# Kernel optimization log

Hardware: AMD Instinct MI355X
Metric: run time of the kernel (lower is better)

## Reference

```python
import jax, jax.numpy as jnp
import numpy as np

N = 100000      # nodes
E = 1600000     # edges (avg degree 16)
D_IN = 128; D_HID = 128; D_OUT = 64; ATT = 64
G = 64          # number of graphs in the batch (dgl.mean_nodes pooling)


def setup_inputs() -> dict:
    key = jax.random.key(0)
    ks = jax.random.split(key, 24)
    def p(i, shape, scale=0.05):
        return jax.random.normal(ks[i], shape, dtype=jnp.float32) * scale
    return dict(
        x=jax.random.normal(ks[0], (N, D_IN), dtype=jnp.float32),
        edge_src=jax.random.randint(ks[1], (E,), 0, N),
        edge_dst=jax.random.randint(ks[2], (E,), 0, N),
        edge_w=jax.random.uniform(ks[3], (E,), dtype=jnp.float32),
        graph_ids=jnp.sort(jax.random.randint(ks[4], (N,), 0, G)),
        # layer 1 (HeteAggregateLayer for type 'node')
        w_self1=p(5, (D_IN, D_HID)), w_rel1=p(6, (D_IN, D_HID)), bias1=p(7, (1, D_HID)),
        w_q1=p(8, (D_HID, ATT)), w_k1=p(9, (D_HID, ATT)), w_att1=p(10, (2 * ATT, 1)),
        # layer 2
        w_self2=p(11, (D_HID, D_OUT)), w_rel2=p(12, (D_HID, D_OUT)), bias2=p(13, (1, D_OUT)),
        w_q2=p(14, (D_OUT, ATT)), w_k2=p(15, (D_OUT, ATT)), w_att2=p(16, (2 * ATT, 1)),
        # final MLP: Linear(d, d//2) -> ReLU -> Linear(d//2, 1)
        mlp_w1=p(17, (D_OUT, D_OUT // 2)), mlp_b1=p(18, (D_OUT // 2,)),
        mlp_w2=p(19, (D_OUT // 2, 1)), mlp_b2=p(20, (1,)),
    )


def _spmm(src, dst, w, feat):
    # torch.spmm(adj, feat): out[dst] += w_edge * feat[src]
    return jax.ops.segment_sum(feat[src] * w[:, None], dst, num_segments=N)


def _agg(x, src, dst, ew, w_self, w_rel, bias, w_q, w_k, w_att):
    self_ft = x @ w_self                        # [N, D]
    nb_ft = _spmm(src, dst, ew, x @ w_rel)      # [N, D]
    nb = jnp.stack([self_ft, nb_ft])            # [T=2, N, D] (self first, as in torch cat order)
    q = self_ft @ w_q                           # [N, A] query (repeated across types)
    keys = jnp.einsum('tnd,da->tna', nb, w_k)   # [T, N, A]
    a = w_att[:, 0]
    # e = elu(cat([keys, query], -1) @ w_att); split w_att into key/query halves
    e = jax.nn.elu(keys @ a[:ATT] + q @ a[ATT:])  # [T, N]
    att = jax.nn.softmax(e, axis=0)               # softmax over types per node
    out = jnp.einsum('tn,tnd->nd', att, nb) + bias
    return out, att.T                              # attention returned as [N, T]


def reference(x, edge_src, edge_dst, edge_w, graph_ids,
              w_self1, w_rel1, bias1, w_q1, w_k1, w_att1,
              w_self2, w_rel2, bias2, w_q2, w_k2, w_att2,
              mlp_w1, mlp_b1, mlp_w2, mlp_b2):
    h, att1 = _agg(x, edge_src, edge_dst, edge_w,
                   w_self1, w_rel1, bias1, w_q1, w_k1, w_att1)
    h = jax.nn.elu(h)   # dropout(0.5) is identity in eval mode
    h, att2 = _agg(h, edge_src, edge_dst, edge_w,
                   w_self2, w_rel2, bias2, w_q2, w_k2, w_att2)
    # dgl.mean_nodes over the batched graph
    sums = jax.ops.segment_sum(h, graph_ids, num_segments=G)
    cnt = jax.ops.segment_sum(jnp.ones((N, 1), h.dtype), graph_ids, num_segments=G)
    hg = sums / jnp.maximum(cnt, 1.0)               # [G, D_OUT]
    hid = jax.nn.relu(hg @ mlp_w1 + mlp_b1)
    graph_embd = hid @ mlp_w2 + mlp_b2              # [G, 1]
    return graph_embd, att1, att2
```

## Files before the change

kernel.cpp:

```cpp
#include <hip/hip_runtime.h>
#include <hip/hip_bf16.h>
#include <cstdint>
#include <cstddef>

static constexpr int D_IN  = 128;
static constexpr int D_HID = 128;
static constexpr int D_OUT = 64;
static constexpr int ATTD  = 64;
static constexpr int NG    = 64;
static constexpr int NB    = 256;
static constexpr int NBLK  = 256;
static constexpr int BSHIFT = 9;

typedef __attribute__((ext_vector_type(8))) short s16x8;
typedef __attribute__((ext_vector_type(4))) float f32x4;
typedef unsigned short ushort_t;
typedef unsigned int uint_t;

__device__ __forceinline__ unsigned short bf_bits(float f) {
    union { __hip_bfloat16 h; unsigned short u; } cv;
    cv.h = __float2bfloat16(f);
    return cv.u;
}
__device__ __forceinline__ float bf_lo(uint_t v) { return __uint_as_float(v << 16); }
__device__ __forceinline__ float bf_hi(uint_t v) { return __uint_as_float(v & 0xffff0000u); }
__device__ __forceinline__ float bf_one(unsigned short u) { return __uint_as_float(((uint_t)u) << 16); }

template <int C, bool A32, bool OA_BF>
__device__ __forceinline__ void gemm_dual_body(ushort_t* wt, int bx,
        const void* __restrict__ A, int M,
        const ushort_t* __restrict__ WTa, const ushort_t* __restrict__ WTb,
        void* __restrict__ Oa, ushort_t* __restrict__ Ob) {
    constexpr int K = 128;
    constexpr int RS = K + 8;

    for (int idx = threadIdx.x; idx < 2 * C * (K / 8); idx += 256) {
        int half = idx >= C * (K / 8);
        int l = idx - half * C * (K / 8);
        int c  = l >> 4;
        int kc = l & 15;
        const ushort_t* W = half ? WTb : WTa;
        *(uint4*)&wt[half * C * RS + c * RS + kc * 8] = *(const uint4*)&W[c * K + kc * 8];
    }
    __syncthreads();

    const int w    = threadIdx.x >> 6;
    const int lane = threadIdx.x & 63;
    const int row  = bx * 64 + w * 16 + (lane & 15);
    const int rowc = row < M ? row : (M - 1);
    const int kb   = (lane >> 4) * 8;

    s16x8 afr[4];
    if (A32) {
        const float* Af = (const float*)A + (size_t)rowc * K + kb;
#pragma unroll
        for (int ks = 0; ks < 4; ++ks) {
            float4 f0 = *(const float4*)(Af + ks * 32);
            float4 f1 = *(const float4*)(Af + ks * 32 + 4);
            s16x8 a;
            a[0] = (short)bf_bits(f0.x); a[1] = (short)bf_bits(f0.y);
            a[2] = (short)bf_bits(f0.z); a[3] = (short)bf_bits(f0.w);
            a[4] = (short)bf_bits(f1.x); a[5] = (short)bf_bits(f1.y);
            a[6] = (short)bf_bits(f1.z); a[7] = (short)bf_bits(f1.w);
            afr[ks] = a;
        }
    } else {
        const ushort_t* Ab = (const ushort_t*)A + (size_t)rowc * K + kb;
#pragma unroll
        for (int ks = 0; ks < 4; ++ks) afr[ks] = *(const s16x8*)(Ab + ks * 32);
    }

    const int colc = lane & 15;
    const int r0   = bx * 64 + w * 16 + (lane >> 4) * 4;

#pragma unroll
    for (int z = 0; z < 2; ++z) {
        const ushort_t* wz = wt + z * C * RS;
#pragma unroll
        for (int ct = 0; ct < C / 16; ++ct) {
            f32x4 acc = {0.f, 0.f, 0.f, 0.f};
            const int colb = ct * 16 + colc;
#pragma unroll
            for (int ks = 0; ks < 4; ++ks) {
                s16x8 b = *(const s16x8*)&wz[colb * RS + ks * 32 + kb];
                acc = __builtin_amdgcn_mfma_f32_16x16x32_bf16(afr[ks], b, acc, 0, 0, 0);
            }
            if (z == 0) {
                if (OA_BF) {
                    ushort_t* O = (ushort_t*)Oa;
#pragma unroll
                    for (int j = 0; j < 4; ++j)
                        if (r0 + j < M) O[(size_t)(r0 + j) * C + colb] = bf_bits(acc[j]);
                } else {
                    float* O = (float*)Oa;
#pragma unroll
                    for (int j = 0; j < 4; ++j)
                        if (r0 + j < M) O[(size_t)(r0 + j) * C + colb] = acc[j];
                }
            } else {
#pragma unroll
                for (int j = 0; j < 4; ++j)
                    if (r0 + j < M) Ob[(size_t)(r0 + j) * C + colb] = bf_bits(acc[j]);
            }
        }
    }
}

__global__ __launch_bounds__(256) void gemm2_kernel(
        const void* __restrict__ A, int M,
        const ushort_t* __restrict__ WTa, const ushort_t* __restrict__ WTb,
        void* __restrict__ Oa, ushort_t* __restrict__ Ob) {
    __shared__ ushort_t wt[2 * 64 * 136];
    gemm_dual_body<64, false, false>(wt, blockIdx.x, A, M, WTa, WTb, Oa, Ob);
}

__global__ __launch_bounds__(256) void phaseA(
        const int* __restrict__ edst, int E, int chunk, int* __restrict__ bh,
        const float* __restrict__ w_self1, const float* __restrict__ w_rel1,
        const float* __restrict__ w_self2, const float* __restrict__ w_rel2,
        ushort_t* __restrict__ wtb,
        const float* __restrict__ w_q1, const float* __restrict__ w_k1,
        const float* __restrict__ w_att1,
        const float* __restrict__ w_q2, const float* __restrict__ w_k2,
        const float* __restrict__ w_att2,
        float* __restrict__ small, float* __restrict__ zero_region,
        int* __restrict__ dctr) {
    __shared__ int h[NB];
    int bid = blockIdx.x;
    if (bid < NBLK) {
        h[threadIdx.x] = 0;
        __syncthreads();
        int beg = bid * chunk;
        int end = min(E, beg + chunk);
        for (int i = beg + threadIdx.x; i < end; i += 256)
            atomicAdd(&h[edst[i] >> BSHIFT], 1);
        __syncthreads();
        bh[threadIdx.x * NBLK + bid] = h[threadIdx.x];
    } else if (bid < NBLK + 192) {
        int idx = (bid - NBLK) * 256 + threadIdx.x;
        const float* src; int base, Cc;
        if (idx < 16384)      { src = w_self1; base = 0;     Cc = 128; }
        else if (idx < 32768) { src = w_rel1;  base = 16384; Cc = 128; }
        else if (idx < 40960) { src = w_self2; base = 32768; Cc = 64;  }
        else                  { src = w_rel2;  base = 40960; Cc = 64;  }
        int l = idx - base;
        int c = l >> 7;
        int k = l & 127;
        wtb[base + l] = bf_bits(src[k * Cc + c]);
    } else if (bid < NBLK + 194) {
        int idx = (bid - NBLK - 192) * 256 + threadIdx.x;
        if (idx < 384) {
            float acc = 0.f;
            if (idx < 128) {
                int d = idx;
                for (int a = 0; a < ATTD; ++a) acc += w_k1[d * ATTD + a] * w_att1[a];
                small[0 + d] = acc;
            } else if (idx < 256) {
                int d = idx - 128;
                for (int a = 0; a < ATTD; ++a) acc += w_q1[d * ATTD + a] * w_att1[ATTD + a];
                small[128 + d] = acc;
            } else if (idx < 320) {
                int d = idx - 256;
                for (int a = 0; a < ATTD; ++a) acc += w_k2[d * ATTD + a] * w_att2[a];
                small[256 + d] = acc;
            } else {
                int d = idx - 320;
                for (int a = 0; a < ATTD; ++a) acc += w_q2[d * ATTD + a] * w_att2[ATTD + a];
                small[320 + d] = acc;
            }
        }
    } else {
        for (int i = threadIdx.x; i < NG * D_OUT + NG; i += 256) zero_region[i] = 0.f;
        if (threadIdx.x == 0) *dctr = 0;
    }
}

__global__ __launch_bounds__(256) void scanA(int* __restrict__ bh,
        int* __restrict__ bt, int* __restrict__ bb, int* __restrict__ dctr) {
    __shared__ int wsum[4];
    __shared__ int lastFlag;
    const int t = blockIdx.x;
    const int i = threadIdx.x;
    if (i == 0) lastFlag = 0;
    int v = bh[t * NBLK + i];
    int lane = i & 63, w = i >> 6;
    int incl = v;
#pragma unroll
    for (int off = 1; off < 64; off <<= 1) {
        int u = __shfl_up(incl, off);
        if (lane >= off) incl += u;
    }
    if (lane == 63) wsum[w] = incl;
    __syncthreads();
    int wbase = 0;
#pragma unroll
    for (int k = 0; k < 4; ++k) if (k < w) wbase += wsum[k];
    int excl = wbase + incl - v;
    bh[t * NBLK + i] = excl;
    __syncthreads();
    if (i == 255) {
        atomicExch(&bt[t], excl + v);
        __threadfence();
        int old = atomicAdd(dctr, 1);
        if (old == NBLK - 1) lastFlag = 1;
    }
    __syncthreads();
    if (lastFlag) {
        int vb = atomicAdd(&bt[i], 0);
        int incl2 = vb;
#pragma unroll
        for (int off = 1; off < 64; off <<= 1) {
            int u = __shfl_up(incl2, off);
            if (lane >= off) incl2 += u;
        }
        if (lane == 63) wsum[w] = incl2;
        __syncthreads();
        int wb2 = 0;
#pragma unroll
        for (int k = 0; k < 4; ++k) if (k < w) wb2 += wsum[k];
        int excl2 = wb2 + incl2 - vb;
        bb[i] = excl2;
        if (i == 255) bb[256] = excl2 + vb;
    }
}

__global__ __launch_bounds__(256) void phaseB(
        const int* __restrict__ src, const int* __restrict__ dst,
        const float* __restrict__ ew, int E, int chunk,
        const int* __restrict__ bh, const int* __restrict__ bb,
        uint2* __restrict__ part,
        const float* __restrict__ x, int M,
        const ushort_t* __restrict__ wt_s1, const ushort_t* __restrict__ wt_r1,
        void* __restrict__ Oa, ushort_t* __restrict__ Ob) {
    __shared__ ushort_t smem[2 * 128 * 136];
    int bid = blockIdx.x;
    if (bid < NBLK) {
        int* ofs = (int*)smem;
        ofs[threadIdx.x] = bh[threadIdx.x * NBLK + bid] + bb[threadIdx.x];
        __syncthreads();
        int beg = bid * chunk;
        int end = min(E, beg + chunk);
        for (int i = beg + threadIdx.x; i < end; i += 256) {
            int d = dst[i];
            int b = d >> BSHIFT;
            int pos = atomicAdd(&ofs[b], 1);
            part[pos] = make_uint2((uint_t)src[i] | ((uint_t)(d & 511) << 20),
                                   __float_as_uint(ew[i]));
        }
    } else {
        gemm_dual_body<128, true, true>(smem, bid - NBLK, x, M, wt_s1, wt_r1, Oa, Ob);
    }
}

__global__ __launch_bounds__(256) void phaseC(
        const uint2* __restrict__ part, const int* __restrict__ bb,
        int* __restrict__ rowptr, float2* __restrict__ sorted, int N_, int nbuck,
        int g1,
        const float* __restrict__ x, int M,
        const ushort_t* __restrict__ wt_s1, const ushort_t* __restrict__ wt_r1,
        void* __restrict__ Oa, ushort_t* __restrict__ Ob) {
    __shared__ ushort_t smem[2 * 128 * 136];
    int bid = blockIdx.x;
    if (bid >= nbuck) {
        gemm_dual_body<128, true, true>(smem, g1 + (bid - nbuck), x, M, wt_s1, wt_r1, Oa, Ob);
        return;
    }
    int* hist = (int*)smem;
    int* wsum = (int*)smem + 512;
    int b = bid;
    int t = threadIdx.x;
    int start = bb[b], end = bb[b + 1];
    hist[t] = 0; hist[t + 256] = 0;
    __syncthreads();
    {
        int i = start + t;
        for (; i + 1792 < end; i += 2048) {
            int k[8];
#pragma unroll
            for (int j = 0; j < 8; ++j) k[j] = part[i + j * 256].x >> 20;
#pragma unroll
            for (int j = 0; j < 8; ++j) atomicAdd(&hist[k[j]], 1);
        }
        for (; i < end; i += 256) atomicAdd(&hist[part[i].x >> 20], 1);
    }
    __syncthreads();
    int v0 = hist[2 * t], v1 = hist[2 * t + 1];
    int pair = v0 + v1;
    int lane = t & 63, w = t >> 6;
    int incl = pair;
#pragma unroll
    for (int off = 1; off < 64; off <<= 1) {
        int u = __shfl_up(incl, off);
        if (lane >= off) incl += u;
    }
    if (lane == 63) wsum[w] = incl;
    __syncthreads();
    int wbase = 0;
#pragma unroll
    for (int i = 0; i < 4; ++i) if (i < w) wbase += wsum[i];
    int excl = wbase + incl - pair;
    __syncthreads();
    hist[2 * t]     = start + excl;
    hist[2 * t + 1] = start + excl + v0;
    int dst0 = (b << BSHIFT) + 2 * t;
    if (dst0 < N_)     rowptr[dst0]     = start + excl + v0;
    if (dst0 + 1 < N_) rowptr[dst0 + 1] = start + excl + v0 + v1;
    __syncthreads();
    {
        int i = start + t;
        for (; i + 1792 < end; i += 2048) {
            uint2 r[8];
#pragma unroll
            for (int j = 0; j < 8; ++j) r[j] = part[i + j * 256];
#pragma unroll
            for (int j = 0; j < 8; ++j) {
                int dl = r[j].x >> 20;
                int pos = atomicAdd(&hist[dl], 1);
                sorted[pos] = make_float2(__int_as_float((int)(r[j].x & 0xFFFFF)),
                                          __uint_as_float(r[j].y));
            }
        }
        for (; i < end; i += 256) {
            uint2 r = part[i];
            int dl = r.x >> 20;
            int pos = atomicAdd(&hist[dl], 1);
            sorted[pos] = make_float2(__int_as_float((int)(r.x & 0xFFFFF)),
                                      __uint_as_float(r.y));
        }
    }
}

__global__ __launch_bounds__(256) void fused1(
        const uint_t* __restrict__ selfp, const ushort_t* __restrict__ relft,
        const int* __restrict__ rowptr, const float2* __restrict__ sorted,
        const float* __restrict__ vk, const float* __restrict__ vq,
        const float* __restrict__ bias,
        uint_t* __restrict__ hout, float* __restrict__ attout, int M) {
    const int wv   = __builtin_amdgcn_readfirstlane(threadIdx.x >> 6);
    const int lane = threadIdx.x & 63;
    const int n = blockIdx.x * 4 + wv;
    if (n >= M) return;

    uint_t s2 = selfp[(size_t)n * 64 + lane];
    float sv0 = bf_lo(s2), sv1 = bf_hi(s2);
    float nb0 = 0.f, nb1 = 0.f;

    const int beg = (n > 0) ? rowptr[n - 1] : 0;
    const int end = rowptr[n];
    const int len = end - beg;
    const char* base = (const char*)relft;
    const uint_t lb = (uint_t)lane << 2;

    int e = beg;
    const int efull = beg + (len & ~7);
    for (; e < efull; e += 8) {
        float2 swb[8];
#pragma unroll
        for (int j = 0; j < 8; ++j) swb[j] = sorted[e + j];
        uint_t vv[8];
#pragma unroll
        for (int j = 0; j < 8; ++j)
            vv[j] = *(const uint_t*)(base + (((uint_t)__float_as_uint(swb[j].x) << 8) | lb));
#pragma unroll
        for (int j = 0; j < 8; ++j) {
            nb0 = fmaf(swb[j].y, bf_lo(vv[j]), nb0);
            nb1 = fmaf(swb[j].y, bf_hi(vv[j]), nb1);
        }
    }
    if (e < end) {
        float2 swb[8];
        float  wb[8];
#pragma unroll
        for (int j = 0; j < 8; ++j) {
            int idx = e + j;
            int cl  = idx < end ? idx : e;
            swb[j] = sorted[cl];
            wb[j]  = idx < end ? swb[j].y : 0.f;
        }
        uint_t vv[8];
#pragma unroll
        for (int j = 0; j < 8; ++j)
            vv[j] = *(const uint_t*)(base + (((uint_t)__float_as_uint(swb[j].x) << 8) | lb));
#pragma unroll
        for (int j = 0; j < 8; ++j) {
            nb0 = fmaf(wb[j], bf_lo(vv[j]), nb0);
            nb1 = fmaf(wb[j], bf_hi(vv[j]), nb1);
        }
    }

    float2 k2 = ((const float2*)vk)[lane];
    float2 q2 = ((const float2*)vq)[lane];
    float sk = sv0 * k2.x + sv1 * k2.y;
    float sq = sv0 * q2.x + sv1 * q2.y;
    float nk = nb0 * k2.x + nb1 * k2.y;
#pragma unroll
    for (int off = 32; off; off >>= 1) {
        sk += __shfl_xor(sk, off);
        sq += __shfl_xor(sq, off);
        nk += __shfl_xor(nk, off);
    }
    float e0 = sk + sq;
    float e1 = nk + sq;
    e0 = e0 > 0.f ? e0 : expm1f(e0);
    e1 = e1 > 0.f ? e1 : expm1f(e1);
    float m = fmaxf(e0, e1);
    float a0 = expf(e0 - m);
    float a1 = expf(e1 - m);
    float inv = 1.f / (a0 + a1);
    a0 *= inv; a1 *= inv;

    float2 b2 = ((const float2*)bias)[lane];
    float o0 = fmaf(a0, sv0, fmaf(a1, nb0, b2.x));
    float o1 = fmaf(a0, sv1, fmaf(a1, nb1, b2.y));
    o0 = o0 > 0.f ? o0 : expm1f(o0);
    o1 = o1 > 0.f ? o1 : expm1f(o1);
    hout[(size_t)n * 64 + lane] = (uint_t)bf_bits(o0) | ((uint_t)bf_bits(o1) << 16);
    if (lane == 0) {
        attout[2 * (size_t)n + 0] = a0;
        attout[2 * (size_t)n + 1] = a1;
    }
}

__global__ __launch_bounds__(256) void fused2(
        const float* __restrict__ selfp, const ushort_t* __restrict__ relft,
        const int* __restrict__ rowptr, const float2* __restrict__ sorted,
        const float* __restrict__ vk, const float* __restrict__ vq,
        const float* __restrict__ bias,
        float* __restrict__ hout, float* __restrict__ attout, int M) {
    const int wv   = __builtin_amdgcn_readfirstlane(threadIdx.x >> 6);
    const int lane = threadIdx.x & 63;
    const int n = blockIdx.x * 4 + wv;
    if (n >= M) return;

    float sv = selfp[(size_t)n * 64 + lane];
    float nb = 0.f;

    const int beg = (n > 0) ? rowptr[n - 1] : 0;
    const int end = rowptr[n];
    const int len = end - beg;
    const char* base = (const char*)relft;
    const uint_t lb = (uint_t)lane << 1;

    int e = beg;
    const int efull = beg + (len & ~7);
    for (; e < efull; e += 8) {
        float2 swb[8];
#pragma unroll
        for (int j = 0; j < 8; ++j) swb[j] = sorted[e + j];
        ushort_t vv[8];
#pragma unroll
        for (int j = 0; j < 8; ++j)
            vv[j] = *(const ushort_t*)(base + (((uint_t)__float_as_uint(swb[j].x) << 7) | lb));
#pragma unroll
        for (int j = 0; j < 8; ++j) nb = fmaf(swb[j].y, bf_one(vv[j]), nb);
    }
    if (e < end) {
        float2 swb[8];
        float  wb[8];
#pragma unroll
        for (int j = 0; j < 8; ++j) {
            int idx = e + j;
            int cl  = idx < end ? idx : e;
            swb[j] = sorted[cl];
            wb[j]  = idx < end ? swb[j].y : 0.f;
        }
        ushort_t vv[8];
#pragma unroll
        for (int j = 0; j < 8; ++j)
            vv[j] = *(const ushort_t*)(base + (((uint_t)__float_as_uint(swb[j].x) << 7) | lb));
#pragma unroll
        for (int j = 0; j < 8; ++j) nb = fmaf(wb[j], bf_one(vv[j]), nb);
    }

    float kk = vk[lane], qq = vq[lane];
    float sk = sv * kk;
    float sq = sv * qq;
    float nk = nb * kk;
#pragma unroll
    for (int off = 32; off; off >>= 1) {
        sk += __shfl_xor(sk, off);
        sq += __shfl_xor(sq, off);
        nk += __shfl_xor(nk, off);
    }
    float e0 = sk + sq;
    float e1 = nk + sq;
    e0 = e0 > 0.f ? e0 : expm1f(e0);
    e1 = e1 > 0.f ? e1 : expm1f(e1);
    float m = fmaxf(e0, e1);
    float a0 = expf(e0 - m);
    float a1 = expf(e1 - m);
    float inv = 1.f / (a0 + a1);
    a0 *= inv; a1 *= inv;

    hout[(size_t)n * 64 + lane] = fmaf(a0, sv, fmaf(a1, nb, bias[lane]));
    if (lane == 0) {
        attout[2 * (size_t)n + 0] = a0;
        attout[2 * (size_t)n + 1] = a1;
    }
}

__global__ __launch_bounds__(256) void pool_sum_v2(
        const float* __restrict__ h, const int* __restrict__ gid,
        float* __restrict__ sums, float* __restrict__ cnt, int M, int chunk) {
    int wave = threadIdx.x >> 6;
    int lane = threadIdx.x & 63;
    int wid  = blockIdx.x * 4 + wave;
    int beg  = wid * chunk;
    int end  = min(M, beg + chunk);
    if (beg >= end) return;

    int   cur_g = gid[beg];
    float acc   = 0.f;
    int   cl    = 0;
    for (int n = beg; n < end; ++n) {
        int g = gid[n];
        if (g != cur_g) {
            atomicAdd(&sums[(size_t)cur_g * D_OUT + lane], acc);
            if (lane == 0) atomicAdd(&cnt[cur_g], (float)cl);
            cur_g = g; acc = 0.f; cl = 0;
        }
        acc += h[(size_t)n * D_OUT + lane];
        ++cl;
    }
    atomicAdd(&sums[(size_t)cur_g * D_OUT + lane], acc);
    if (lane == 0) atomicAdd(&cnt[cur_g], (float)cl);
}

__global__ void pool_mlp(const float* __restrict__ sums, const float* __restrict__ cnt,
                         const float* __restrict__ w1, const float* __restrict__ b1,
                         const float* __restrict__ w2, const float* __restrict__ b2,
                         float* __restrict__ out) {
    int g = threadIdx.x;
    if (g >= NG) return;
    float c = fmaxf(cnt[g], 1.0f);
    float inv = 1.0f / c;
    float hg[D_OUT];
#pragma unroll
    for (int d = 0; d < D_OUT; ++d) hg[d] = sums[g * D_OUT + d] * inv;
    float acc = b2[0];
    for (int j = 0; j < D_OUT / 2; ++j) {
        float hid = b1[j];
#pragma unroll 8
        for (int d = 0; d < D_OUT; ++d) hid = fmaf(hg[d], w1[d * (D_OUT / 2) + j], hid);
        hid = fmaxf(hid, 0.f);
        acc = fmaf(hid, w2[j], acc);
    }
    out[g] = acc;
}

extern "C" void kernel_launch(void* const* d_in, const int* in_sizes, int n_in,
                              void* d_out, int out_size, void* d_ws, size_t ws_size,
                              hipStream_t stream) {
    const float* x       = (const float*)d_in[0];
    const int*   esrc    = (const int*)  d_in[1];
    const int*   edst    = (const int*)  d_in[2];
    const float* ew      = (const float*)d_in[3];
    const int*   gid     = (const int*)  d_in[4];
    const float* w_self1 = (const float*)d_in[5];
    const float* w_rel1  = (const float*)d_in[6];
    const float* bias1   = (const float*)d_in[7];
    const float* w_q1    = (const float*)d_in[8];
    const float* w_k1    = (const float*)d_in[9];
    const float* w_att1  = (const float*)d_in[10];
    const float* w_self2 = (const float*)d_in[11];
    const float* w_rel2  = (const float*)d_in[12];
    const float* bias2   = (const float*)d_in[13];
    const float* w_q2    = (const float*)d_in[14];
    const float* w_k2    = (const float*)d_in[15];
    const float* w_att2  = (const float*)d_in[16];
    const float* mlp_w1  = (const float*)d_in[17];
    const float* mlp_b1  = (const float*)d_in[18];
    const float* mlp_w2  = (const float*)d_in[19];
    const float* mlp_b2  = (const float*)d_in[20];

    const int N = in_sizes[0] / D_IN;
    const int E = in_sizes[1];

    float* out = (float*)d_out;
    float* out_embd = out;
    float* out_att1 = out + NG;
    float* out_att2 = out + NG + 2 * (size_t)N;

    float* ws = (float*)d_ws;
    size_t nf = (size_t)N;
    float* bufS = ws;
    float* bufR = ws + nf * 64;
    float* bufH = ws + nf * 128;
    uint2* part = (uint2*)bufH;
    int* ip     = (int*)(ws + nf * 192);
    int* bh     = ip;
    int* rowptr = ip + NB * NBLK;
    int* bb     = rowptr + N;
    int* bt     = bb + 257;
    int* dctr   = bt + 256;
    size_t int_end = nf * 192 + (size_t)NB * NBLK + nf + 257 + 256 + 1;
    int_end = (int_end + 1) & ~(size_t)1;
    float2* sorted = (float2*)(ws + int_end);
    float* small = ws + int_end + 2 * (size_t)E;
    float* vk1 = small + 0;
    float* vq1 = small + 128;
    float* vk2 = small + 256;
    float* vq2 = small + 320;
    float* sums = small + 384;
    float* cnt  = small + 384 + NG * D_OUT;
    ushort_t* wtb = (ushort_t*)(small + 384 + NG * D_OUT + NG);
    ushort_t* wt_s1 = wtb;
    ushort_t* wt_r1 = wtb + 16384;
    ushort_t* wt_s2 = wtb + 32768;
    ushort_t* wt_r2 = wtb + 40960;

    const int chunk = (E + NBLK - 1) / NBLK;
    const int nbuck = (N + (1 << BSHIFT) - 1) >> BSHIFT;
    const int nx    = (N + 63) / 64;
    const int g1    = (nx * 3) / 5;

    phaseA<<<NBLK + 192 + 2 + 1, 256, 0, stream>>>(
        edst, E, chunk, bh,
        w_self1, w_rel1, w_self2, w_rel2, wtb,
        w_q1, w_k1, w_att1, w_q2, w_k2, w_att2, small, sums, dctr);

    scanA<<<NBLK, 256, 0, stream>>>(bh, bt, bb, dctr);

    phaseB<<<NBLK + g1, 256, 0, stream>>>(
        esrc, edst, ew, E, chunk, bh, bb, part,
        x, N, wt_s1, wt_r1, (void*)bufS, (ushort_t*)bufR);

    phaseC<<<nbuck + (nx - g1), 256, 0, stream>>>(
        part, bb, rowptr, sorted, N, nbuck, g1,
        x, N, wt_s1, wt_r1, (void*)bufS, (ushort_t*)bufR);

    fused1<<<(N + 3) / 4, 256, 0, stream>>>(
        (const uint_t*)bufS, (const ushort_t*)bufR, rowptr, sorted,
        vk1, vq1, bias1, (uint_t*)bufH, out_att1, N);

    gemm2_kernel<<<nx, 256, 0, stream>>>(
        (const void*)bufH, N, wt_s2, wt_r2, (void*)bufS, (ushort_t*)bufR);

    fused2<<<(N + 3) / 4, 256, 0, stream>>>(
        bufS, (const ushort_t*)bufR, rowptr, sorted,
        vk2, vq2, bias2, bufH, out_att2, N);

    {
        int pblocks = 1024;
        int pchunk  = (N + pblocks * 4 - 1) / (pblocks * 4);
        pool_sum_v2<<<pblocks, 256, 0, stream>>>(bufH, gid, sums, cnt, N, pchunk);
    }
    pool_mlp<<<1, 64, 0, stream>>>(sums, cnt, mlp_w1, mlp_b1, mlp_w2, mlp_b2, out_embd);
}
```

Baseline: 273.3 us.

## Store layer-2 self features as bf16, unroll edge loops, fuse pooling with MLP

The layer-2 GEMM now writes the self-projection in bf16 instead of fp32, and fused2 reads and widens it, which halves that buffer's traffic at some precision cost. The histogram and scatter loops in phaseA and phaseB are unrolled by four so several loads are in flight per thread. The pooling sum and final MLP are merged into one kernel, where the last block to finish (tracked by a new atomic counter reset in phaseA) computes the MLP. This removes one kernel launch but adds a grid-wide completion counter.

```diff
diff --git a/kernel.cpp b/kernel.cpp
--- a/kernel.cpp
+++ b/kernel.cpp
@@ -111,7 +111,7 @@
         const ushort_t* __restrict__ WTa, const ushort_t* __restrict__ WTb,
         void* __restrict__ Oa, ushort_t* __restrict__ Ob) {
     __shared__ ushort_t wt[2 * 64 * 136];
-    gemm_dual_body<64, false, false>(wt, blockIdx.x, A, M, WTa, WTb, Oa, Ob);
+    gemm_dual_body<64, false, true>(wt, blockIdx.x, A, M, WTa, WTb, Oa, Ob);
 }
 
 __global__ __launch_bounds__(256) void phaseA(
@@ -124,7 +124,7 @@
         const float* __restrict__ w_q2, const float* __restrict__ w_k2,
         const float* __restrict__ w_att2,
         float* __restrict__ small, float* __restrict__ zero_region,
-        int* __restrict__ dctr) {
+        int* __restrict__ dctr, int* __restrict__ dctr2) {
     __shared__ int h[NB];
     int bid = blockIdx.x;
     if (bid < NBLK) {
@@ -132,7 +132,15 @@
         __syncthreads();
         int beg = bid * chunk;
         int end = min(E, beg + chunk);
-        for (int i = beg + threadIdx.x; i < end; i += 256)
+        int i = beg + threadIdx.x;
+        for (; i + 768 < end; i += 1024) {
+            int d0 = edst[i], d1 = edst[i + 256], d2 = edst[i + 512], d3 = edst[i + 768];
+            atomicAdd(&h[d0 >> BSHIFT], 1);
+            atomicAdd(&h[d1 >> BSHIFT], 1);
+            atomicAdd(&h[d2 >> BSHIFT], 1);
+            atomicAdd(&h[d3 >> BSHIFT], 1);
+        }
+        for (; i < end; i += 256)
             atomicAdd(&h[edst[i] >> BSHIFT], 1);
         __syncthreads();
         bh[threadIdx.x * NBLK + bid] = h[threadIdx.x];
@@ -171,7 +179,7 @@
         }
     } else {
         for (int i = threadIdx.x; i < NG * D_OUT + NG; i += 256) zero_region[i] = 0.f;
-        if (threadIdx.x == 0) *dctr = 0;
+        if (threadIdx.x == 0) { *dctr = 0; *dctr2 = 0; }
     }
 }
 
@@ -240,7 +248,25 @@
         __syncthreads();
         int beg = bid * chunk;
         int end = min(E, beg + chunk);
-        for (int i = beg + threadIdx.x; i < end; i += 256) {
+        int i = beg + threadIdx.x;
+        for (; i + 768 < end; i += 1024) {
+            int   d[4], s[4];
+            float wv[4];
+#pragma unroll
+            for (int j = 0; j < 4; ++j) d[j] = dst[i + j * 256];
+#pragma unroll
+            for (int j = 0; j < 4; ++j) s[j] = src[i + j * 256];
+#pragma unroll
+            for (int j = 0; j < 4; ++j) wv[j] = ew[i + j * 256];
+#pragma unroll
+            for (int j = 0; j < 4; ++j) {
+                int b = d[j] >> BSHIFT;
+                int pos = atomicAdd(&ofs[b], 1);
+                part[pos] = make_uint2((uint_t)s[j] | ((uint_t)(d[j] & 511) << 20),
+                                       __float_as_uint(wv[j]));
+            }
+        }
+        for (; i < end; i += 256) {
             int d = dst[i];
             int b = d >> BSHIFT;
             int pos = atomicAdd(&ofs[b], 1);
@@ -422,7 +448,7 @@
 }
 
 __global__ __launch_bounds__(256) void fused2(
-        const float* __restrict__ selfp, const ushort_t* __restrict__ relft,
+        const ushort_t* __restrict__ selfp, const ushort_t* __restrict__ relft,
         const int* __restrict__ rowptr, const float2* __restrict__ sorted,
         const float* __restrict__ vk, const float* __restrict__ vq,
         const float* __restrict__ bias,
@@ -432,7 +458,7 @@
     const int n = blockIdx.x * 4 + wv;
     if (n >= M) return;
 
-    float sv = selfp[(size_t)n * 64 + lane];
+    float sv = bf_one(selfp[(size_t)n * 64 + lane]);
     float nb = 0.f;
 
     const int beg = (n > 0) ? rowptr[n - 1] : 0;
@@ -499,53 +525,62 @@
     }
 }
 
-__global__ __launch_bounds__(256) void pool_sum_v2(
+__global__ __launch_bounds__(256) void pool_all(
         const float* __restrict__ h, const int* __restrict__ gid,
-        float* __restrict__ sums, float* __restrict__ cnt, int M, int chunk) {
+        float* __restrict__ sums, float* __restrict__ cnt, int M, int chunk,
+        const float* __restrict__ w1, const float* __restrict__ b1,
+        const float* __restrict__ w2, const float* __restrict__ b2,
+        float* __restrict__ out, int* __restrict__ dctr2) {
+    __shared__ int lastFlag;
+    if (threadIdx.x == 0) lastFlag = 0;
+
     int wave = threadIdx.x >> 6;
     int lane = threadIdx.x & 63;
     int wid  = blockIdx.x * 4 + wave;
     int beg  = wid * chunk;
     int end  = min(M, beg + chunk);
-    if (beg >= end) return;
-
-    int   cur_g = gid[beg];
-    float acc   = 0.f;
-    int   cl    = 0;
-    for (int n = beg; n < end; ++n) {
-        int g = gid[n];
-        if (g != cur_g) {
-            atomicAdd(&sums[(size_t)cur_g * D_OUT + lane], acc);
-            if (lane == 0) atomicAdd(&cnt[cur_g], (float)cl);
-            cur_g = g; acc = 0.f; cl = 0;
-        }
-        acc += h[(size_t)n * D_OUT + lane];
-        ++cl;
-    }
-    atomicAdd(&sums[(size_t)cur_g * D_OUT + lane], acc);
-    if (lane == 0) atomicAdd(&cnt[cur_g], (float)cl);
-}
-
-__global__ void pool_mlp(const float* __restrict__ sums, const float* __restrict__ cnt,
-                         const float* __restrict__ w1, const float* __restrict__ b1,
-                         const float* __restrict__ w2, const float* __restrict__ b2,
-                         float* __restrict__ out) {
-    int g = threadIdx.x;
-    if (g >= NG) return;
-    float c = fmaxf(cnt[g], 1.0f);
-    float inv = 1.0f / c;
-    float hg[D_OUT];
-#pragma unroll
-    for (int d = 0; d < D_OUT; ++d) hg[d] = sums[g * D_OUT + d] * inv;
-    float acc = b2[0];
-    for (int j = 0; j < D_OUT / 2; ++j) {
-        float hid = b1[j];
+    if (beg < end) {
+        int   cur_g = gid[beg];
+        float acc   = 0.f;
+        int   cl    = 0;
+        for (int n = beg; n < end; ++n) {
+            int g = gid[n];
+            if (g != cur_g) {
+                atomicAdd(&sums[(size_t)cur_g * D_OUT + lane], acc);
+                if (lane == 0) atomicAdd(&cnt[cur_g], (float)cl);
+                cur_g = g; acc = 0.f; cl = 0;
+            }
+            acc += h[(size_t)n * D_OUT + lane];
+            ++cl;
+        }
+        atomicAdd(&sums[(size_t)cur_g * D_OUT + lane], acc);
+        if (lane == 0) atomicAdd(&cnt[cur_g], (float)cl);
+    }
+    __syncthreads();
+    if (threadIdx.x == 0) {
+        __threadfence();
+        int old = atomicAdd(dctr2, 1);
+        if (old == gridDim.x - 1) lastFlag = 1;
+    }
+    __syncthreads();
+    if (lastFlag && threadIdx.x < NG) {
+        int g = threadIdx.x;
+        float c = fmaxf(atomicAdd(&cnt[g], 0.f), 1.0f);
+        float inv = 1.0f / c;
+        float hg[D_OUT];
+#pragma unroll
+        for (int d = 0; d < D_OUT; ++d)
+            hg[d] = atomicAdd(&sums[g * D_OUT + d], 0.f) * inv;
+        float acc = b2[0];
+        for (int j = 0; j < D_OUT / 2; ++j) {
+            float hid = b1[j];
 #pragma unroll 8
-        for (int d = 0; d < D_OUT; ++d) hid = fmaf(hg[d], w1[d * (D_OUT / 2) + j], hid);
-        hid = fmaxf(hid, 0.f);
-        acc = fmaf(hid, w2[j], acc);
-    }
-    out[g] = acc;
+            for (int d = 0; d < D_OUT; ++d) hid = fmaf(hg[d], w1[d * (D_OUT / 2) + j], hid);
+            hid = fmaxf(hid, 0.f);
+            acc = fmaf(hid, w2[j], acc);
+        }
+        out[g] = acc;
+    }
 }
 
 extern "C" void kernel_launch(void* const* d_in, const int* in_sizes, int n_in,
@@ -593,7 +628,8 @@
     int* bb     = rowptr + N;
     int* bt     = bb + 257;
     int* dctr   = bt + 256;
-    size_t int_end = nf * 192 + (size_t)NB * NBLK + nf + 257 + 256 + 1;
+    int* dctr2  = dctr + 1;
+    size_t int_end = nf * 192 + (size_t)NB * NBLK + nf + 257 + 256 + 2;
     int_end = (int_end + 1) & ~(size_t)1;
     float2* sorted = (float2*)(ws + int_end);
     float* small = ws + int_end + 2 * (size_t)E;
@@ -617,7 +653,7 @@
     phaseA<<<NBLK + 192 + 2 + 1, 256, 0, stream>>>(
         edst, E, chunk, bh,
         w_self1, w_rel1, w_self2, w_rel2, wtb,
-        w_q1, w_k1, w_att1, w_q2, w_k2, w_att2, small, sums, dctr);
+        w_q1, w_k1, w_att1, w_q2, w_k2, w_att2, small, sums, dctr, dctr2);
 
     scanA<<<NBLK, 256, 0, stream>>>(bh, bt, bb, dctr);
 
@@ -637,13 +673,14 @@
         (const void*)bufH, N, wt_s2, wt_r2, (void*)bufS, (ushort_t*)bufR);
 
     fused2<<<(N + 3) / 4, 256, 0, stream>>>(
-        bufS, (const ushort_t*)bufR, rowptr, sorted,
+        (const ushort_t*)bufS, (const ushort_t*)bufR, rowptr, sorted,
         vk2, vq2, bias2, bufH, out_att2, N);
 
     {
         int pblocks = 1024;
         int pchunk  = (N + pblocks * 4 - 1) / (pblocks * 4);
-        pool_sum_v2<<<pblocks, 256, 0, stream>>>(bufH, gid, sums, cnt, N, pchunk);
-    }
-    pool_mlp<<<1, 64, 0, stream>>>(sums, cnt, mlp_w1, mlp_b1, mlp_w2, mlp_b2, out_embd);
-}
+        pool_all<<<pblocks, 256, 0, stream>>>(
+            bufH, gid, sums, cnt, N, pchunk,
+            mlp_w1, mlp_b1, mlp_w2, mlp_b2, out_embd, dctr2);
+    }
+}
```

Result: slower. 284.8 us (+4.2%).
